# Performance work log

Hardware: AMD Instinct MI355X
Metric: run time of the kernel (lower is better)

Reference implementation:

```python
import jax, jax.numpy as jnp
import numpy as np

K, T, V = 64, 100, 10000
DELTA = 0.005
EPS_DIV = 1e-6


def setup_inputs() -> dict:
    key = jax.random.key(0)
    k1, k2, k3 = jax.random.split(key, 3)
    mu_q_beta = jax.random.normal(k1, (K, T, V), dtype=jnp.float32)
    logsig_q_beta = jax.random.normal(k2, (K, T, V), dtype=jnp.float32)
    eps = jax.random.normal(k3, (T, K, V), dtype=jnp.float32)  # randn_like noise for reparameterize
    return {"mu_q_beta": mu_q_beta, "logsig_q_beta": logsig_q_beta, "eps": eps}


def reference(mu_q_beta, logsig_q_beta, eps):
    # Rearrange params from [K, T, V] to the time-major layout [T, K, V]
    mu = jnp.transpose(mu_q_beta, (1, 0, 2))
    ls = jnp.transpose(logsig_q_beta, (1, 0, 2))

    # reparameterize: beta[t] = mu[t] + exp(0.5 * logsig[t]) * eps[t]
    # (beta[t] has no dependency on beta[t-1] -> fully vectorized over T)
    betas = mu + jnp.exp(0.5 * ls) * eps  # [T, K, V]

    # KL at t=0 against N(0, I): p_logsigma = 0 -> sigma_p_sq = 1
    kl0 = 0.5 * jnp.sum((jnp.exp(ls[0]) + mu[0] ** 2) / (1.0 + EPS_DIV) - 1.0 - ls[0])

    # KL at t>=1 against N(beta[t-1], delta): sigma_p_sq = delta, p_logsigma = log(delta)
    log_delta = jnp.log(jnp.float32(DELTA))
    diff = mu[1:] - betas[:-1]  # one-step lag prior mean
    kl_rest = 0.5 * jnp.sum(
        (jnp.exp(ls[1:]) + diff ** 2) / (DELTA + EPS_DIV) - 1.0 + log_delta - ls[1:]
    )

    kl_beta = kl0 + kl_rest
    return jax.nn.softmax(betas, axis=-1), kl_beta
```

## Files before the change

### kernel.cpp

```cpp
#include <hip/hip_runtime.h>
#include <math.h>

#define KDIM 64
#define TDIM 100
#define VDIM 10000
#define NV4  2500
#define BLOCK 512
#define NWAVE (BLOCK / 64)
#define VPT 5
#define CHUNK 5
#define NCHUNK (TDIM / CHUNK)

#define INV1 (1.0f / (1.0f + 1e-6f))
#define INVD (1.0f / (0.005f + 1e-6f))
#define LOGD (-5.2983173665480363f)

typedef float vf4 __attribute__((ext_vector_type(4)));

#define INRANGE(jj, idx) ((jj) < VPT - 1 || (idx) < NV4)

__device__ __forceinline__ float wave_red_sum(float v) {
#pragma unroll
    for (int m = 32; m >= 1; m >>= 1) v += __shfl_xor(v, m, 64);
    return v;
}

__device__ __forceinline__ void lds_barrier() {
    asm volatile("s_waitcnt lgkmcnt(0)\n\ts_barrier" ::: "memory");
}

__global__ __launch_bounds__(BLOCK, 4) void fused_beta_softmax_kl(
    const float* __restrict__ mu_q,
    const float* __restrict__ lsq,
    const float* __restrict__ eps,
    float* __restrict__ out,
    float* __restrict__ kl)
{
    __shared__ vf4 bprev[NV4];
    __shared__ float red[2][NWAVE];
    __shared__ float kred[NWAVE];

    const int tid = threadIdx.x;
    const int bid = blockIdx.x;
    const int k   = bid / NCHUNK;
    const int c   = bid % NCHUNK;
    const int t0  = c * CHUNK;
    const int tend = t0 + CHUNK;
    const bool epi = (tend < TDIM);

    float klacc = 0.0f;
    vf4 M[VPT], L[VPT], E[VPT];

    {
        const size_t po = ((size_t)k * TDIM + t0) * VDIM;
        const size_t eo = ((size_t)t0 * KDIM + k) * VDIM;
        const vf4* m4p = reinterpret_cast<const vf4*>(mu_q + po);
        const vf4* l4p = reinterpret_cast<const vf4*>(lsq + po);
        const vf4* e4p = reinterpret_cast<const vf4*>(eps + eo);
#pragma unroll
        for (int jj = 0; jj < VPT; ++jj) {
            const int idx = tid + jj * BLOCK;
            if (INRANGE(jj, idx)) {
                M[jj] = m4p[idx];
                L[jj] = l4p[idx];
                E[jj] = __builtin_nontemporal_load(&e4p[idx]);
            }
        }
    }

    for (int t = t0; t < tend; ++t) {
        const bool first = (t == 0);
        const bool skip  = (t == t0) && (t0 != 0);

        float lsum = 0.0f;
#pragma unroll
        for (int jj = 0; jj < VPT; ++jj) {
            const int idx = tid + jj * BLOCK;
            if (INRANGE(jj, idx)) {
                const vf4 m = M[jj], l = L[jj], e = E[jj];
                const float sx = __expf(0.5f * l.x), sy = __expf(0.5f * l.y),
                            sz = __expf(0.5f * l.z), sw = __expf(0.5f * l.w);
                vf4 b;
                b.x = fmaf(sx, e.x, m.x);
                b.y = fmaf(sy, e.y, m.y);
                b.z = fmaf(sz, e.z, m.z);
                b.w = fmaf(sw, e.w, m.w);
                if (first) {
                    klacc += (sx * sx + m.x * m.x) * INV1 - 1.0f - l.x;
                    klacc += (sy * sy + m.y * m.y) * INV1 - 1.0f - l.y;
                    klacc += (sz * sz + m.z * m.z) * INV1 - 1.0f - l.z;
                    klacc += (sw * sw + m.w * m.w) * INV1 - 1.0f - l.w;
                } else if (!skip) {
                    const vf4 p = bprev[idx];
                    const float dx = m.x - p.x, dy = m.y - p.y,
                                dz = m.z - p.z, dw = m.w - p.w;
                    klacc += (sx * sx + dx * dx) * INVD - 1.0f + LOGD - l.x;
                    klacc += (sy * sy + dy * dy) * INVD - 1.0f + LOGD - l.y;
                    klacc += (sz * sz + dz * dz) * INVD - 1.0f + LOGD - l.z;
                    klacc += (sw * sw + dw * dw) * INVD - 1.0f + LOGD - l.w;
                }
                bprev[idx] = b;
                lsum += __expf(b.x) + __expf(b.y) + __expf(b.z) + __expf(b.w);
            }
        }

        if (t + 1 < tend) {
            const size_t po = ((size_t)k * TDIM + (t + 1)) * VDIM;
            const size_t eo = ((size_t)(t + 1) * KDIM + k) * VDIM;
            const vf4* m4p = reinterpret_cast<const vf4*>(mu_q + po);
            const vf4* l4p = reinterpret_cast<const vf4*>(lsq + po);
            const vf4* e4p = reinterpret_cast<const vf4*>(eps + eo);
#pragma unroll
            for (int jj = 0; jj < VPT; ++jj) {
                const int idx = tid + jj * BLOCK;
                if (INRANGE(jj, idx)) {
                    M[jj] = m4p[idx];
                    L[jj] = l4p[idx];
                    E[jj] = __builtin_nontemporal_load(&e4p[idx]);
                }
            }
        } else if (epi) {
            const size_t po = ((size_t)k * TDIM + tend) * VDIM;
            const vf4* m4p = reinterpret_cast<const vf4*>(mu_q + po);
            const vf4* l4p = reinterpret_cast<const vf4*>(lsq + po);
#pragma unroll
            for (int jj = 0; jj < VPT; ++jj) {
                const int idx = tid + jj * BLOCK;
                if (INRANGE(jj, idx)) { M[jj] = m4p[idx]; L[jj] = l4p[idx]; }
            }
        }

        const int slot = t & 1;
        float ws = wave_red_sum(lsum);
        if ((tid & 63) == 0) red[slot][tid >> 6] = ws;
        lds_barrier();
        float rowsum = 0.0f;
#pragma unroll
        for (int w = 0; w < NWAVE; ++w) rowsum += red[slot][w];
        const float invs = 1.0f / rowsum;

        vf4* o4p = reinterpret_cast<vf4*>(out + ((size_t)t * KDIM + k) * VDIM);
#pragma unroll
        for (int jj = 0; jj < VPT; ++jj) {
            const int idx = tid + jj * BLOCK;
            if (INRANGE(jj, idx)) {
                const vf4 b = bprev[idx];
                vf4 o;
                o.x = __expf(b.x) * invs;
                o.y = __expf(b.y) * invs;
                o.z = __expf(b.z) * invs;
                o.w = __expf(b.w) * invs;
                __builtin_nontemporal_store(o, &o4p[idx]);
            }
        }
    }

    if (epi) {
#pragma unroll
        for (int jj = 0; jj < VPT; ++jj) {
            const int idx = tid + jj * BLOCK;
            if (INRANGE(jj, idx)) {
                const vf4 m = M[jj], l = L[jj];
                const vf4 p = bprev[idx];
                const float sx = __expf(0.5f * l.x), sy = __expf(0.5f * l.y),
                            sz = __expf(0.5f * l.z), sw = __expf(0.5f * l.w);
                const float dx = m.x - p.x, dy = m.y - p.y,
                            dz = m.z - p.z, dw = m.w - p.w;
                klacc += (sx * sx + dx * dx) * INVD - 1.0f + LOGD - l.x;
                klacc += (sy * sy + dy * dy) * INVD - 1.0f + LOGD - l.y;
                klacc += (sz * sz + dz * dz) * INVD - 1.0f + LOGD - l.z;
                klacc += (sw * sw + dw * dw) * INVD - 1.0f + LOGD - l.w;
            }
        }
    }

    float wk = wave_red_sum(klacc);
    __syncthreads();
    if ((tid & 63) == 0) kred[tid >> 6] = wk;
    __syncthreads();
    if (tid == 0) {
        float tot = 0.0f;
#pragma unroll
        for (int w = 0; w < NWAVE; ++w) tot += kred[w];
        atomicAdd(kl, 0.5f * tot);
    }
}

extern "C" void kernel_launch(void* const* d_in, const int* in_sizes, int n_in,
                              void* d_out, int out_size, void* d_ws, size_t ws_size,
                              hipStream_t stream) {
    const float* mu_q = (const float*)d_in[0];
    const float* lsq  = (const float*)d_in[1];
    const float* eps  = (const float*)d_in[2];
    float* out = (float*)d_out;
    float* kl  = out + (size_t)TDIM * KDIM * VDIM;

    (void)hipMemsetAsync(kl, 0, sizeof(float), stream);

    dim3 grid(KDIM * NCHUNK);
    fused_beta_softmax_kl<<<grid, BLOCK, 0, stream>>>(mu_q, lsq, eps, out, kl);
}
```

Before: 205.9 us.

## Stage inputs via async global-to-LDS DMA with double-buffered halves

Replaces register prefetch of mu/logsig/eps with global_load_lds asynchronous copies into two LDS half-row stages, refilling each half as soon as it is consumed so that loads for the next timestep overlap compute and stores. The previous beta is kept in registers instead of an LDS array, and the block grows to 640 threads so four vf4 slots cover the row. This aims to hide memory latency and cut register pressure, at the cost of much larger LDS use (about 120KB per block), which limits occupancy to roughly one block per CU, plus hand-written vmcnt waits that depend on exact load counts.

```diff
diff --git a/kernel.cpp b/kernel.cpp
--- a/kernel.cpp
+++ b/kernel.cpp
@@ -5,11 +5,12 @@
 #define TDIM 100
 #define VDIM 10000
 #define NV4  2500
-#define BLOCK 512
-#define NWAVE (BLOCK / 64)
-#define VPT 5
+#define BLOCK 640
+#define NWAVE 10
+#define HALFS 1280
 #define CHUNK 5
 #define NCHUNK (TDIM / CHUNK)
+#define TAIL  (NV4 - 3 * BLOCK)
 
 #define INV1 (1.0f / (1.0f + 1e-6f))
 #define INVD (1.0f / (0.005f + 1e-6f))
@@ -17,26 +18,85 @@
 
 typedef float vf4 __attribute__((ext_vector_type(4)));
 
-#define INRANGE(jj, idx) ((jj) < VPT - 1 || (idx) < NV4)
-
 __device__ __forceinline__ float wave_red_sum(float v) {
 #pragma unroll
     for (int m = 32; m >= 1; m >>= 1) v += __shfl_xor(v, m, 64);
     return v;
 }
 
+__device__ __forceinline__ void async16(const vf4* g, vf4* l) {
+    __builtin_amdgcn_global_load_lds(
+        (const __attribute__((address_space(1))) void*)(const void*)g,
+        (__attribute__((address_space(3))) void*)(void*)l, 16, 0, 0);
+}
+
+__device__ __forceinline__ void waitv6() { asm volatile("s_waitcnt vmcnt(6)" ::: "memory"); }
+__device__ __forceinline__ void waitv0() { asm volatile("s_waitcnt vmcnt(0)" ::: "memory"); }
+__device__ __forceinline__ void raw_barrier() { asm volatile("s_barrier" ::: "memory"); }
 __device__ __forceinline__ void lds_barrier() {
     asm volatile("s_waitcnt lgkmcnt(0)\n\ts_barrier" ::: "memory");
 }
 
-__global__ __launch_bounds__(BLOCK, 4) void fused_beta_softmax_kl(
+template <int HR>
+__device__ __forceinline__ void dma_half(const float* mu_row, const float* ls_row,
+                                         const float* ep_row, vf4* st, int tid) {
+#pragma unroll
+    for (int j = 0; j < 2; ++j) {
+        const int s    = tid + j * BLOCK;
+        const int slot = HR * HALFS + s;
+        if (HR == 0 || slot < NV4) {
+            async16((const vf4*)mu_row + slot, st + 0 * HALFS + s);
+            async16((const vf4*)ls_row + slot, st + 1 * HALFS + s);
+            async16((const vf4*)ep_row + slot, st + 2 * HALFS + s);
+        }
+    }
+}
+
+__device__ __forceinline__ void consume(const vf4 m, const vf4 l, const vf4 e,
+                                        vf4& B, const bool first, const bool skip,
+                                        float& klacc, float& lsum) {
+    const float sx = __expf(0.5f * l.x), sy = __expf(0.5f * l.y),
+                sz = __expf(0.5f * l.z), sw = __expf(0.5f * l.w);
+    vf4 b;
+    b.x = fmaf(sx, e.x, m.x);
+    b.y = fmaf(sy, e.y, m.y);
+    b.z = fmaf(sz, e.z, m.z);
+    b.w = fmaf(sw, e.w, m.w);
+    if (first) {
+        klacc += (sx * sx + m.x * m.x) * INV1 - 1.0f - l.x;
+        klacc += (sy * sy + m.y * m.y) * INV1 - 1.0f - l.y;
+        klacc += (sz * sz + m.z * m.z) * INV1 - 1.0f - l.z;
+        klacc += (sw * sw + m.w * m.w) * INV1 - 1.0f - l.w;
+    } else if (!skip) {
+        const float dx = m.x - B.x, dy = m.y - B.y, dz = m.z - B.z, dw = m.w - B.w;
+        klacc += (sx * sx + dx * dx) * INVD - 1.0f + LOGD - l.x;
+        klacc += (sy * sy + dy * dy) * INVD - 1.0f + LOGD - l.y;
+        klacc += (sz * sz + dz * dz) * INVD - 1.0f + LOGD - l.z;
+        klacc += (sw * sw + dw * dw) * INVD - 1.0f + LOGD - l.w;
+    }
+    B = b;
+    lsum += __expf(b.x) + __expf(b.y) + __expf(b.z) + __expf(b.w);
+}
+
+__device__ __forceinline__ void kl_step(const vf4 m, const vf4 l, const vf4 B,
+                                        float& klacc) {
+    const float sx = __expf(0.5f * l.x), sy = __expf(0.5f * l.y),
+                sz = __expf(0.5f * l.z), sw = __expf(0.5f * l.w);
+    const float dx = m.x - B.x, dy = m.y - B.y, dz = m.z - B.z, dw = m.w - B.w;
+    klacc += (sx * sx + dx * dx) * INVD - 1.0f + LOGD - l.x;
+    klacc += (sy * sy + dy * dy) * INVD - 1.0f + LOGD - l.y;
+    klacc += (sz * sz + dz * dz) * INVD - 1.0f + LOGD - l.z;
+    klacc += (sw * sw + dw * dw) * INVD - 1.0f + LOGD - l.w;
+}
+
+__global__ __launch_bounds__(BLOCK) void fused_beta_softmax_kl(
     const float* __restrict__ mu_q,
     const float* __restrict__ lsq,
     const float* __restrict__ eps,
     float* __restrict__ out,
     float* __restrict__ kl)
 {
-    __shared__ vf4 bprev[NV4];
+    __shared__ vf4 stage[2][3 * HALFS];
     __shared__ float red[2][NWAVE];
     __shared__ float kred[NWAVE];
 
@@ -49,129 +109,90 @@
     const bool epi = (tend < TDIM);
 
     float klacc = 0.0f;
-    vf4 M[VPT], L[VPT], E[VPT];
-
-    {
-        const size_t po = ((size_t)k * TDIM + t0) * VDIM;
-        const size_t eo = ((size_t)t0 * KDIM + k) * VDIM;
-        const vf4* m4p = reinterpret_cast<const vf4*>(mu_q + po);
-        const vf4* l4p = reinterpret_cast<const vf4*>(lsq + po);
-        const vf4* e4p = reinterpret_cast<const vf4*>(eps + eo);
-#pragma unroll
-        for (int jj = 0; jj < VPT; ++jj) {
-            const int idx = tid + jj * BLOCK;
-            if (INRANGE(jj, idx)) {
-                M[jj] = m4p[idx];
-                L[jj] = l4p[idx];
-                E[jj] = __builtin_nontemporal_load(&e4p[idx]);
+    vf4 B0, B1, B2, B3;
+
+    const float* mu_row = mu_q + ((size_t)k * TDIM + t0) * VDIM;
+    const float* ls_row = lsq  + ((size_t)k * TDIM + t0) * VDIM;
+    const float* ep_row = eps  + ((size_t)t0 * KDIM + k) * VDIM;
+
+    dma_half<0>(mu_row, ls_row, ep_row, stage[0], tid);
+    dma_half<1>(mu_row, ls_row, ep_row, stage[1], tid);
+
+    for (int r = 0; r < CHUNK; ++r) {
+        const int t = t0 + r;
+        const bool first = (t == 0);
+        const bool skip  = (r == 0) && (t0 != 0);
+        const bool more  = (r + 1 < CHUNK);
+        const float* mu_n = mu_row + VDIM;
+        const float* ls_n = ls_row + VDIM;
+        const float* ep_n = ep_row + (size_t)KDIM * VDIM;
+        float lsum = 0.0f;
+
+        waitv6();
+        raw_barrier();
+        {
+            const vf4* S = stage[0];
+            const vf4 m0 = S[tid],          l0 = S[HALFS + tid],          e0 = S[2 * HALFS + tid];
+            const vf4 m1 = S[tid + BLOCK],  l1 = S[HALFS + tid + BLOCK],  e1 = S[2 * HALFS + tid + BLOCK];
+            consume(m0, l0, e0, B0, first, skip, klacc, lsum);
+            consume(m1, l1, e1, B1, first, skip, klacc, lsum);
+        }
+        lds_barrier();
+        if (more) dma_half<0>(mu_n, ls_n, ep_n, stage[0], tid);
+
+        if (more) waitv6(); else waitv0();
+        raw_barrier();
+        {
+            const vf4* S = stage[1];
+            const vf4 m0 = S[tid],         l0 = S[HALFS + tid],         e0 = S[2 * HALFS + tid];
+            consume(m0, l0, e0, B2, first, skip, klacc, lsum);
+            if (tid < TAIL) {
+                const vf4 m1 = S[tid + BLOCK], l1 = S[HALFS + tid + BLOCK], e1 = S[2 * HALFS + tid + BLOCK];
+                consume(m1, l1, e1, B3, first, skip, klacc, lsum);
             }
         }
-    }
-
-    for (int t = t0; t < tend; ++t) {
-        const bool first = (t == 0);
-        const bool skip  = (t == t0) && (t0 != 0);
-
-        float lsum = 0.0f;
-#pragma unroll
-        for (int jj = 0; jj < VPT; ++jj) {
-            const int idx = tid + jj * BLOCK;
-            if (INRANGE(jj, idx)) {
-                const vf4 m = M[jj], l = L[jj], e = E[jj];
-                const float sx = __expf(0.5f * l.x), sy = __expf(0.5f * l.y),
-                            sz = __expf(0.5f * l.z), sw = __expf(0.5f * l.w);
-                vf4 b;
-                b.x = fmaf(sx, e.x, m.x);
-                b.y = fmaf(sy, e.y, m.y);
-                b.z = fmaf(sz, e.z, m.z);
-                b.w = fmaf(sw, e.w, m.w);
-                if (first) {
-                    klacc += (sx * sx + m.x * m.x) * INV1 - 1.0f - l.x;
-                    klacc += (sy * sy + m.y * m.y) * INV1 - 1.0f - l.y;
-                    klacc += (sz * sz + m.z * m.z) * INV1 - 1.0f - l.z;
-                    klacc += (sw * sw + m.w * m.w) * INV1 - 1.0f - l.w;
-                } else if (!skip) {
-                    const vf4 p = bprev[idx];
-                    const float dx = m.x - p.x, dy = m.y - p.y,
-                                dz = m.z - p.z, dw = m.w - p.w;
-                    klacc += (sx * sx + dx * dx) * INVD - 1.0f + LOGD - l.x;
-                    klacc += (sy * sy + dy * dy) * INVD - 1.0f + LOGD - l.y;
-                    klacc += (sz * sz + dz * dz) * INVD - 1.0f + LOGD - l.z;
-                    klacc += (sw * sw + dw * dw) * INVD - 1.0f + LOGD - l.w;
-                }
-                bprev[idx] = b;
-                lsum += __expf(b.x) + __expf(b.y) + __expf(b.z) + __expf(b.w);
-            }
-        }
-
-        if (t + 1 < tend) {
-            const size_t po = ((size_t)k * TDIM + (t + 1)) * VDIM;
-            const size_t eo = ((size_t)(t + 1) * KDIM + k) * VDIM;
-            const vf4* m4p = reinterpret_cast<const vf4*>(mu_q + po);
-            const vf4* l4p = reinterpret_cast<const vf4*>(lsq + po);
-            const vf4* e4p = reinterpret_cast<const vf4*>(eps + eo);
-#pragma unroll
-            for (int jj = 0; jj < VPT; ++jj) {
-                const int idx = tid + jj * BLOCK;
-                if (INRANGE(jj, idx)) {
-                    M[jj] = m4p[idx];
-                    L[jj] = l4p[idx];
-                    E[jj] = __builtin_nontemporal_load(&e4p[idx]);
-                }
-            }
-        } else if (epi) {
-            const size_t po = ((size_t)k * TDIM + tend) * VDIM;
-            const vf4* m4p = reinterpret_cast<const vf4*>(mu_q + po);
-            const vf4* l4p = reinterpret_cast<const vf4*>(lsq + po);
-#pragma unroll
-            for (int jj = 0; jj < VPT; ++jj) {
-                const int idx = tid + jj * BLOCK;
-                if (INRANGE(jj, idx)) { M[jj] = m4p[idx]; L[jj] = l4p[idx]; }
-            }
-        }
-
-        const int slot = t & 1;
+
         float ws = wave_red_sum(lsum);
-        if ((tid & 63) == 0) red[slot][tid >> 6] = ws;
+        if ((tid & 63) == 0) red[r & 1][tid >> 6] = ws;
         lds_barrier();
         float rowsum = 0.0f;
 #pragma unroll
-        for (int w = 0; w < NWAVE; ++w) rowsum += red[slot][w];
+        for (int w = 0; w < NWAVE; ++w) rowsum += red[r & 1][w];
         const float invs = 1.0f / rowsum;
 
         vf4* o4p = reinterpret_cast<vf4*>(out + ((size_t)t * KDIM + k) * VDIM);
-#pragma unroll
-        for (int jj = 0; jj < VPT; ++jj) {
-            const int idx = tid + jj * BLOCK;
-            if (INRANGE(jj, idx)) {
-                const vf4 b = bprev[idx];
-                vf4 o;
-                o.x = __expf(b.x) * invs;
-                o.y = __expf(b.y) * invs;
-                o.z = __expf(b.z) * invs;
-                o.w = __expf(b.w) * invs;
-                __builtin_nontemporal_store(o, &o4p[idx]);
+        {
+            vf4 o;
+            o.x = __expf(B0.x) * invs; o.y = __expf(B0.y) * invs;
+            o.z = __expf(B0.z) * invs; o.w = __expf(B0.w) * invs;
+            __builtin_nontemporal_store(o, &o4p[tid]);
+            o.x = __expf(B1.x) * invs; o.y = __expf(B1.y) * invs;
+            o.z = __expf(B1.z) * invs; o.w = __expf(B1.w) * invs;
+            __builtin_nontemporal_store(o, &o4p[tid + BLOCK]);
+            o.x = __expf(B2.x) * invs; o.y = __expf(B2.y) * invs;
+            o.z = __expf(B2.z) * invs; o.w = __expf(B2.w) * invs;
+            __builtin_nontemporal_store(o, &o4p[HALFS + tid]);
+            if (tid < TAIL) {
+                o.x = __expf(B3.x) * invs; o.y = __expf(B3.y) * invs;
+                o.z = __expf(B3.z) * invs; o.w = __expf(B3.w) * invs;
+                __builtin_nontemporal_store(o, &o4p[HALFS + tid + BLOCK]);
             }
         }
+        if (more) dma_half<1>(mu_n, ls_n, ep_n, stage[1], tid);
+
+        mu_row = mu_n; ls_row = ls_n; ep_row = ep_n;
     }
 
     if (epi) {
-#pragma unroll
-        for (int jj = 0; jj < VPT; ++jj) {
-            const int idx = tid + jj * BLOCK;
-            if (INRANGE(jj, idx)) {
-                const vf4 m = M[jj], l = L[jj];
-                const vf4 p = bprev[idx];
-                const float sx = __expf(0.5f * l.x), sy = __expf(0.5f * l.y),
-                            sz = __expf(0.5f * l.z), sw = __expf(0.5f * l.w);
-                const float dx = m.x - p.x, dy = m.y - p.y,
-                            dz = m.z - p.z, dw = m.w - p.w;
-                klacc += (sx * sx + dx * dx) * INVD - 1.0f + LOGD - l.x;
-                klacc += (sy * sy + dy * dy) * INVD - 1.0f + LOGD - l.y;
-                klacc += (sz * sz + dz * dz) * INVD - 1.0f + LOGD - l.z;
-                klacc += (sw * sw + dw * dw) * INVD - 1.0f + LOGD - l.w;
-            }
-        }
+        const float* mu_e = mu_q + ((size_t)k * TDIM + tend) * VDIM;
+        const float* ls_e = lsq  + ((size_t)k * TDIM + tend) * VDIM;
+        const vf4* m4p = (const vf4*)mu_e;
+        const vf4* l4p = (const vf4*)ls_e;
+        kl_step(m4p[tid], l4p[tid], B0, klacc);
+        kl_step(m4p[tid + BLOCK], l4p[tid + BLOCK], B1, klacc);
+        kl_step(m4p[HALFS + tid], l4p[HALFS + tid], B2, klacc);
+        if (tid < TAIL)
+            kl_step(m4p[HALFS + tid + BLOCK], l4p[HALFS + tid + BLOCK], B3, klacc);
     }
 
     float wk = wave_red_sum(klacc);
```

Measured after the change: 211.8 us. 1.03x slower.
